# Kernel tuning notes

Measured on AMD Instinct MI355X. Metric: run time of the kernel, lower is better.

## Reference

```python
import jax, jax.numpy as jnp
import numpy as np
from jax import lax

B, H, W, C = 16, 256, 256, 1
LOC_C = 31            # channels out of localization network
BN_EPS = 1e-3         # Keras BatchNormalization default epsilon
NEG_SLOPE = 0.1       # LeakyReLU slope


def _conv_relu(x, k, b):
    y = lax.conv_general_dilated(x, k, (1, 1), 'SAME',
                                 dimension_numbers=('NHWC', 'HWIO', 'NHWC'))
    return jax.nn.relu(y + b)


def _maxpool2(x):
    return lax.reduce_window(x, -jnp.inf, lax.max, (1, 2, 2, 1), (1, 2, 2, 1), 'VALID')


def _resize_nearest(x, out_h, out_w):
    # tf.image.resize(..., method='nearest') with half-pixel centers
    b, h, w, c = x.shape
    ih = jnp.floor((jnp.arange(out_h) + 0.5) * h / out_h).astype(jnp.int32)
    iw = jnp.floor((jnp.arange(out_w) + 0.5) * w / out_w).astype(jnp.int32)
    return x[:, ih][:, :, iw]


def _generate_grid(theta, height, width):
    # base grid in [-1, 1], x varies along width, y along height
    xs = jnp.arange(width, dtype=jnp.float32) / (width - 1) * 2.0 - 1.0
    ys = jnp.arange(height, dtype=jnp.float32) / (height - 1) * 2.0 - 1.0
    gx, gy = jnp.meshgrid(xs, ys)                      # (H, W)
    grid = jnp.stack([gx, gy], axis=-1).reshape(height * width, 2)  # (HW, 2)
    th = theta.reshape(-1, 2, 3)
    A = th[:, :, :2]                                   # (B, 2, 2)
    t = th[:, :, 2]                                    # (B, 2)
    # NOTE: source does grid @ A (not A @ grid) -- replicate exactly
    tg = jnp.einsum('nc,bcd->bnd', grid, A) + t[:, None, :]
    return tg.reshape(-1, height, width, 2)


def _sampler(img, grid):
    b, h, w, c = img.shape
    x = 0.5 * ((grid[..., 0] + 1.0) * (w - 1))
    y = 0.5 * ((grid[..., 1] + 1.0) * (h - 1))
    x0 = jnp.floor(x); x1 = x0 + 1.0
    y0 = jnp.floor(y); y1 = y0 + 1.0
    x0 = jnp.clip(x0, 0.0, w - 1.0); x1 = jnp.clip(x1, 0.0, w - 1.0)
    y0 = jnp.clip(y0, 0.0, h - 1.0); y1 = jnp.clip(y1, 0.0, h - 1.0)
    wa = (x1 - x) * (y1 - y)
    wb = (x1 - x) * (y - y0)
    wc = (x - x0) * (y1 - y)
    wd = (x - x0) * (y - y0)
    xi0 = x0.astype(jnp.int32); xi1 = x1.astype(jnp.int32)
    yi0 = y0.astype(jnp.int32); yi1 = y1.astype(jnp.int32)
    img_flat = img.reshape(b, h * w, c)

    def gather(yi, xi):
        idx = (yi * w + xi).reshape(b, h * w, 1)       # (B, HW, 1)
        return jnp.take_along_axis(img_flat, idx, axis=1).reshape(b, h, w, c)

    Ia = gather(yi0, xi0)
    Ib = gather(yi1, xi0)
    Ic = gather(yi0, xi1)
    Id = gather(yi1, xi1)
    return (wa[..., None] * Ia + wb[..., None] * Ib
            + wc[..., None] * Ic + wd[..., None] * Id)


def setup_inputs() -> dict:
    key = jax.random.key(0)
    ks = jax.random.split(key, 16)
    s = 0.05
    feat = (H // 8) * (W // 8) * LOC_C  # 31744 flattened localization features
    return {
        'x': jax.random.normal(ks[0], (B, H, W, C), jnp.float32),
        'conv1_k': jax.random.normal(ks[1], (3, 3, C, 8), jnp.float32) * s,
        'conv1_b': jnp.zeros((8,), jnp.float32),
        'conv2_k': jax.random.normal(ks[2], (3, 3, 8, 16), jnp.float32) * s,
        'conv2_b': jnp.zeros((16,), jnp.float32),
        'conv3_k': jax.random.normal(ks[3], (3, 3, 16, LOC_C), jnp.float32) * s,
        'conv3_b': jnp.zeros((LOC_C,), jnp.float32),
        'bn_gamma': 1.0 + 0.1 * jax.random.normal(ks[4], (feat,), jnp.float32),
        'bn_beta': 0.1 * jax.random.normal(ks[5], (feat,), jnp.float32),
        'bn_mean': jnp.zeros((feat,), jnp.float32),
        'bn_var': jnp.ones((feat,), jnp.float32),
        'd1_k': jax.random.normal(ks[6], (feat, 64), jnp.float32) * 0.01,
        'd1_b': jnp.zeros((64,), jnp.float32),
        'd2_k': jax.random.normal(ks[7], (64, 96), jnp.float32) * s,
        'd2_b': jnp.zeros((96,), jnp.float32),
        'd3_k': jax.random.normal(ks[8], (96, 6), jnp.float32) * 0.01,
        'd3_b': jnp.array([1, 0, 0, 0, 1, 0], jnp.float32),
    }


def reference(x, conv1_k, conv1_b, conv2_k, conv2_b, conv3_k, conv3_b,
              bn_gamma, bn_beta, bn_mean, bn_var,
              d1_k, d1_b, d2_k, d2_b, d3_k, d3_b):
    # localization network: (conv-relu, pool) x3 -> (B, H/8, W/8, 31)
    xi = _maxpool2(_conv_relu(x, conv1_k, conv1_b))
    xi = _maxpool2(_conv_relu(xi, conv2_k, conv2_b))
    x_intermediate = _maxpool2(_conv_relu(xi, conv3_k, conv3_b))
    # transformation parameter network (BN in inference mode, dropout = identity)
    f = x_intermediate.reshape(x.shape[0], -1)
    f = (f - bn_mean) * jax.lax.rsqrt(bn_var + BN_EPS) * bn_gamma + bn_beta
    f = jax.nn.relu(f @ d1_k + d1_b)
    f = jax.nn.relu(f @ d2_k + d2_b)
    theta = f @ d3_k + d3_b                            # (B, 6)
    grid = _generate_grid(theta, H, W)                 # (B, H, W, 2)
    loc_up = _resize_nearest(x_intermediate, H, W)     # (B, H, W, 31)
    xc = jnp.concatenate([x, loc_up], axis=-1)         # (B, H, W, 32)
    out = _sampler(xc, grid)
    return jnp.where(out >= 0, out, NEG_SLOPE * out)
```

## Files before the change

kernel.cpp:

```cpp
#include <hip/hip_runtime.h>


#define NEG_SLOPE 0.1f
#define BN_EPS 1e-3f

__global__ __launch_bounds__(256) void st_conv1(const float* __restrict__ x,
                                                const float* __restrict__ w,
                                                const float* __restrict__ bias,
                                                float* __restrict__ outA) {
    int idx = blockIdx.x * 256 + threadIdx.x;
    int px = idx & 127, py = (idx >> 7) & 127, b = idx >> 14;
    const float* xb = x + b * 65536;
    int iy0 = 2 * py - 1, ix0 = 2 * px - 1;
    float p[16];
#pragma unroll
    for (int r = 0; r < 4; ++r) {
        int iy = iy0 + r;
        bool oky = (iy >= 0) && (iy < 256);
#pragma unroll
        for (int cc = 0; cc < 4; ++cc) {
            int ix = ix0 + cc;
            bool ok = oky && (ix >= 0) && (ix < 256);
            p[r * 4 + cc] = ok ? xb[iy * 256 + ix] : 0.0f;
        }
    }
    float m[8];
#pragma unroll
    for (int co = 0; co < 8; ++co) m[co] = -1e30f;
#pragma unroll
    for (int oy = 0; oy < 2; ++oy)
#pragma unroll
        for (int ox = 0; ox < 2; ++ox) {
            float acc[8];
#pragma unroll
            for (int co = 0; co < 8; ++co) acc[co] = 0.0f;
#pragma unroll
            for (int ky = 0; ky < 3; ++ky)
#pragma unroll
                for (int kx = 0; kx < 3; ++kx) {
                    float pv = p[(oy + ky) * 4 + (ox + kx)];
                    const float* wr = w + (ky * 3 + kx) * 8;
#pragma unroll
                    for (int co = 0; co < 8; ++co)
                        acc[co] = fmaf(pv, wr[co], acc[co]);
                }
#pragma unroll
            for (int co = 0; co < 8; ++co) m[co] = fmaxf(m[co], acc[co]);
        }
    float* o = outA + idx * 8;
#pragma unroll
    for (int co = 0; co < 8; ++co) {
        float v = m[co] + bias[co];
        o[co] = v > 0.0f ? v : 0.0f;
    }
}

__global__ __launch_bounds__(256) void st_conv2(const float* __restrict__ A,
                                                const float* __restrict__ w,
                                                const float* __restrict__ bias,
                                                float* __restrict__ outB) {
    int idx = blockIdx.x * 256 + threadIdx.x;
    int half = idx & 1;
    int pixel = idx >> 1;
    int px = pixel & 63, py = (pixel >> 6) & 63, b = pixel >> 12;
    const float* Ab = A + b * 128 * 128 * 8;
    int iy0 = 2 * py - 1, ix0 = 2 * px - 1;
    int cobase = half * 8;
    float acc[4][8];
#pragma unroll
    for (int pos = 0; pos < 4; ++pos)
#pragma unroll
        for (int co = 0; co < 8; ++co) acc[pos][co] = 0.0f;

    for (int ci = 0; ci < 8; ++ci) {
        float p[16];
#pragma unroll
        for (int r = 0; r < 4; ++r) {
            int iy = iy0 + r;
            bool oky = (iy >= 0) && (iy < 128);
#pragma unroll
            for (int cc = 0; cc < 4; ++cc) {
                int ix = ix0 + cc;
                bool ok = oky && (ix >= 0) && (ix < 128);
                p[r * 4 + cc] = ok ? Ab[(iy * 128 + ix) * 8 + ci] : 0.0f;
            }
        }
#pragma unroll
        for (int ky = 0; ky < 3; ++ky)
#pragma unroll
            for (int kx = 0; kx < 3; ++kx) {
                const float* wr = w + ((ky * 3 + kx) * 8 + ci) * 16 + cobase;
                float p00 = p[ky * 4 + kx];
                float p01 = p[ky * 4 + kx + 1];
                float p10 = p[(ky + 1) * 4 + kx];
                float p11 = p[(ky + 1) * 4 + kx + 1];
#pragma unroll
                for (int co = 0; co < 8; ++co) {
                    float wv = wr[co];
                    acc[0][co] = fmaf(p00, wv, acc[0][co]);
                    acc[1][co] = fmaf(p01, wv, acc[1][co]);
                    acc[2][co] = fmaf(p10, wv, acc[2][co]);
                    acc[3][co] = fmaf(p11, wv, acc[3][co]);
                }
            }
    }
    float* o = outB + pixel * 16 + cobase;
#pragma unroll
    for (int co = 0; co < 8; ++co) {
        float m = fmaxf(fmaxf(acc[0][co], acc[1][co]),
                        fmaxf(acc[2][co], acc[3][co]));
        m += bias[cobase + co];
        o[co] = m > 0.0f ? m : 0.0f;
    }
}

__global__ __launch_bounds__(256) void st_conv3(const float* __restrict__ Bf,
                                                const float* __restrict__ w,
                                                const float* __restrict__ bias,
                                                float* __restrict__ outC) {
    int idx = blockIdx.x * 256 + threadIdx.x;
    int q = idx & 3;
    int pixel = idx >> 2;
    int ix = pixel & 63, iy = (pixel >> 6) & 63, b = pixel >> 12;
    int cobase = q * 8;
    if (cobase > 23) cobase = 23;
    const float* Bb = Bf + b * 64 * 64 * 16;
    float acc[8];
#pragma unroll
    for (int co = 0; co < 8; ++co) acc[co] = 0.0f;

    for (int ci = 0; ci < 16; ++ci) {
        float p[9];
#pragma unroll
        for (int ky = 0; ky < 3; ++ky) {
            int y = iy + ky - 1;
            bool oky = (y >= 0) && (y < 64);
#pragma unroll
            for (int kx = 0; kx < 3; ++kx) {
                int xx = ix + kx - 1;
                bool ok = oky && (xx >= 0) && (xx < 64);
                p[ky * 3 + kx] = ok ? Bb[(y * 64 + xx) * 16 + ci] : 0.0f;
            }
        }
#pragma unroll
        for (int k = 0; k < 9; ++k) {
            float pv = p[k];
            const float* wr = w + (k * 16 + ci) * 31 + cobase;
#pragma unroll
            for (int co = 0; co < 8; ++co)
                acc[co] = fmaf(pv, wr[co], acc[co]);
        }
    }
    float* o = outC + pixel * 31 + cobase;
#pragma unroll
    for (int co = 0; co < 8; ++co) {
        float v = acc[co] + bias[cobase + co];
        o[co] = v > 0.0f ? v : 0.0f;
    }
}

__global__ __launch_bounds__(256) void st_pool3(const float* __restrict__ C3,
                                                const float* __restrict__ gamma,
                                                const float* __restrict__ beta,
                                                const float* __restrict__ mean,
                                                const float* __restrict__ var,
                                                float* __restrict__ xip,
                                                float* __restrict__ fprime) {
    int idx = blockIdx.x * 256 + threadIdx.x;
    unsigned j = (unsigned)idx % 31744u;
    unsigned b = (unsigned)idx / 31744u;
    unsigned p2 = j / 31u;
    unsigned co = j - p2 * 31u;
    unsigned px = p2 & 31u, py = p2 >> 5;
    const float* Cb = C3 + b * 64 * 64 * 31;
    float m = -1e30f;
#pragma unroll
    for (int dy = 0; dy < 2; ++dy)
#pragma unroll
        for (int dx = 0; dx < 2; ++dx)
            m = fmaxf(m, Cb[((2 * py + dy) * 64 + (2 * px + dx)) * 31 + co]);
    xip[((b << 10) + p2) * 32 + 1 + co] = m;
    float sc = gamma[j] * rsqrtf(var[j] + BN_EPS);
    fprime[idx] = (m - mean[j]) * sc + beta[j];
}

__global__ __launch_bounds__(256) void st_d1(const float* __restrict__ fp,
                                             const float* __restrict__ k1,
                                             float* __restrict__ partial) {
    int o = blockIdx.x;
    int slice = blockIdx.y;
    int t = threadIdx.x;
    float acc[16];
#pragma unroll
    for (int b = 0; b < 16; ++b) acc[b] = 0.0f;
    int jend = (slice + 1) * 1984;
    for (int j = slice * 1984 + t; j < jend; j += 256) {
        float kv = k1[j * 64 + o];
#pragma unroll
        for (int b = 0; b < 16; ++b)
            acc[b] = fmaf(fp[b * 31744 + j], kv, acc[b]);
    }
#pragma unroll
    for (int b = 0; b < 16; ++b) {
        float v = acc[b];
#pragma unroll
        for (int off = 32; off > 0; off >>= 1) v += __shfl_down(v, off, 64);
        acc[b] = v;
    }
    __shared__ float red[4][16];
    int wave = t >> 6, lane = t & 63;
    if (lane == 0) {
#pragma unroll
        for (int b = 0; b < 16; ++b) red[wave][b] = acc[b];
    }
    __syncthreads();
    if (t < 16) {
        float s = red[0][t] + red[1][t] + red[2][t] + red[3][t];
        partial[(o * 16 + slice) * 16 + t] = s;
    }
}

__global__ __launch_bounds__(256) void st_d1b(const float* __restrict__ partial,
                                              const float* __restrict__ bias,
                                              float* __restrict__ h1) {
    int gid = blockIdx.x * 256 + threadIdx.x;
    int o = gid >> 4, b = gid & 15;
    float s = 0.0f;
#pragma unroll
    for (int sl = 0; sl < 16; ++sl) s += partial[(o * 16 + sl) * 16 + b];
    s += bias[o];
    h1[b * 64 + o] = s > 0.0f ? s : 0.0f;
}

__global__ __launch_bounds__(128) void st_theta(const float* __restrict__ h1,
                                                const float* __restrict__ k2,
                                                const float* __restrict__ b2,
                                                const float* __restrict__ k3,
                                                const float* __restrict__ b3,
                                                float* __restrict__ theta) {
    int b = blockIdx.x, t = threadIdx.x;
    __shared__ float h2[96];
    if (t < 96) {
        float s = b2[t];
        for (int i = 0; i < 64; ++i) s = fmaf(h1[b * 64 + i], k2[i * 96 + t], s);
        h2[t] = s > 0.0f ? s : 0.0f;
    }
    __syncthreads();
    if (t < 6) {
        float s = b3[t];
        for (int i = 0; i < 96; ++i) s = fmaf(h2[i], k3[i * 6 + t], s);
        theta[b * 6 + t] = s;
    }
}

__global__ __launch_bounds__(256) void st_sample(const float* __restrict__ x,
                                                 const float* __restrict__ xip,
                                                 const float* __restrict__ theta,
                                                 float* __restrict__ out) {
    __shared__ float smem[256 * 33];
    int t = threadIdx.x;
    int p = blockIdx.x * 256 + t;
    int ow = p & 255, oh = (p >> 8) & 255;
    int b = blockIdx.x >> 8;

    const float* th = theta + b * 6;
    float t0 = th[0], t1 = th[1], t2 = th[2], t3 = th[3], t4 = th[4], t5 = th[5];
    float gx = (float)ow * (2.0f / 255.0f) - 1.0f;
    float gy = (float)oh * (2.0f / 255.0f) - 1.0f;
    float sx = gx * t0 + gy * t3 + t2;
    float sy = gx * t1 + gy * t4 + t5;
    float xf = 0.5f * ((sx + 1.0f) * 255.0f);
    float yf = 0.5f * ((sy + 1.0f) * 255.0f);
    float x0 = floorf(xf), y0 = floorf(yf);
    float x1 = x0 + 1.0f, y1 = y0 + 1.0f;
    x0 = fminf(fmaxf(x0, 0.0f), 255.0f);
    x1 = fminf(fmaxf(x1, 0.0f), 255.0f);
    y0 = fminf(fmaxf(y0, 0.0f), 255.0f);
    y1 = fminf(fmaxf(y1, 0.0f), 255.0f);
    float wa = (x1 - xf) * (y1 - yf);
    float wb = (x1 - xf) * (yf - y0);
    float wc = (xf - x0) * (y1 - yf);
    float wd = (xf - x0) * (yf - y0);
    int xi0 = (int)x0, xi1 = (int)x1, yi0 = (int)y0, yi1 = (int)y1;

    const float* xb = x + b * 65536;
    float Ia = xb[yi0 * 256 + xi0];
    float Ib = xb[yi1 * 256 + xi0];
    float Ic = xb[yi0 * 256 + xi1];
    float Id = xb[yi1 * 256 + xi1];
    float fine = wa * Ia + wb * Ib + wc * Ic + wd * Id;
    fine = fine >= 0.0f ? fine : NEG_SLOPE * fine;

    const float* cellbase = xip + (b << 15);
    const float4* pa = (const float4*)(cellbase + (((yi0 >> 3) << 5) + (xi0 >> 3)) * 32);
    const float4* pb = (const float4*)(cellbase + (((yi1 >> 3) << 5) + (xi0 >> 3)) * 32);
    const float4* pc = (const float4*)(cellbase + (((yi0 >> 3) << 5) + (xi1 >> 3)) * 32);
    const float4* pd = (const float4*)(cellbase + (((yi1 >> 3) << 5) + (xi1 >> 3)) * 32);

    int sbase = t * 33;
#pragma unroll
    for (int k = 0; k < 8; ++k) {
        float4 va = pa[k], vb = pb[k], vc = pc[k], vd = pd[k];
        float vx = fmaf(wa, va.x, fmaf(wb, vb.x, fmaf(wc, vc.x, wd * vd.x)));
        float vy = fmaf(wa, va.y, fmaf(wb, vb.y, fmaf(wc, vc.y, wd * vd.y)));
        float vz = fmaf(wa, va.z, fmaf(wb, vb.z, fmaf(wc, vc.z, wd * vd.z)));
        float vw = fmaf(wa, va.w, fmaf(wb, vb.w, fmaf(wc, vc.w, wd * vd.w)));
        vx = vx >= 0.0f ? vx : NEG_SLOPE * vx;
        vy = vy >= 0.0f ? vy : NEG_SLOPE * vy;
        vz = vz >= 0.0f ? vz : NEG_SLOPE * vz;
        vw = vw >= 0.0f ? vw : NEG_SLOPE * vw;
        if (k == 0) vx = fine;
        smem[sbase + 4 * k]     = vx;
        smem[sbase + 4 * k + 1] = vy;
        smem[sbase + 4 * k + 2] = vz;
        smem[sbase + 4 * k + 3] = vw;
    }
    __syncthreads();

    float* ob = out + blockIdx.x * 8192;
#pragma unroll
    for (int i = 0; i < 32; ++i) {
        int idx = i * 256 + t;
        ob[idx] = smem[(idx >> 5) * 33 + (idx & 31)];
    }
}

extern "C" void kernel_launch(void* const* d_in, const int* in_sizes, int n_in,
                              void* d_out, int out_size, void* d_ws, size_t ws_size,
                              hipStream_t stream) {
    const float* x     = (const float*)d_in[0];
    const float* c1k   = (const float*)d_in[1];
    const float* c1b   = (const float*)d_in[2];
    const float* c2k   = (const float*)d_in[3];
    const float* c2b   = (const float*)d_in[4];
    const float* c3k   = (const float*)d_in[5];
    const float* c3b   = (const float*)d_in[6];
    const float* gamma = (const float*)d_in[7];
    const float* beta  = (const float*)d_in[8];
    const float* mean  = (const float*)d_in[9];
    const float* var   = (const float*)d_in[10];
    const float* d1k   = (const float*)d_in[11];
    const float* d1b   = (const float*)d_in[12];
    const float* d2k   = (const float*)d_in[13];
    const float* d2b   = (const float*)d_in[14];
    const float* d3k   = (const float*)d_in[15];
    const float* d3b   = (const float*)d_in[16];
    float* out = (float*)d_out;
    float* ws  = (float*)d_ws;

    float* A       = ws;
    float* Bf      = ws + 2097152;
    float* C3      = ws;
    float* xip     = ws + 2097152;
    float* fprime  = ws + 2097152 + 524288;
    float* partial = ws + 3145728;
    float* h1      = ws + 3145728 + 16384;
    float* theta   = ws + 3145728 + 17408;

    st_conv1<<<1024, 256, 0, stream>>>(x, c1k, c1b, A);
    st_conv2<<<512, 256, 0, stream>>>(A, c2k, c2b, Bf);
    st_conv3<<<1024, 256, 0, stream>>>(Bf, c3k, c3b, C3);
    st_pool3<<<1984, 256, 0, stream>>>(C3, gamma, beta, mean, var, xip, fprime);
    st_d1<<<dim3(64, 16), 256, 0, stream>>>(fprime, d1k, partial);
    st_d1b<<<4, 256, 0, stream>>>(partial, d1b, h1);
    st_theta<<<16, 128, 0, stream>>>(h1, d2k, d2b, d3k, d3b, theta);
    st_sample<<<4096, 256, 0, stream>>>(x, xip, theta, out);
}
```

Before: 309.4 us.

## Vectorize conv and pool loads, pad conv3 output, restructure dense1 and sampler stores

```diff
diff --git a/kernel.cpp b/kernel.cpp
--- a/kernel.cpp
+++ b/kernel.cpp
@@ -4,10 +4,18 @@
 #define NEG_SLOPE 0.1f
 #define BN_EPS 1e-3f
 
-__global__ __launch_bounds__(256) void st_conv1(const float* __restrict__ x,
-                                                const float* __restrict__ w,
-                                                const float* __restrict__ bias,
-                                                float* __restrict__ outA) {
+typedef float vfloat4 __attribute__((ext_vector_type(4)));
+
+__device__ __forceinline__ void fma8(float pv, const float* __restrict__ wk,
+                                     float* __restrict__ acc) {
+#pragma unroll
+    for (int co = 0; co < 8; ++co) acc[co] = fmaf(pv, wk[co], acc[co]);
+}
+
+__global__ __launch_bounds__(256, 4) void st_conv1(const float* __restrict__ x,
+                                                   const float* __restrict__ w,
+                                                   const float* __restrict__ bias,
+                                                   float* __restrict__ outA) {
     int idx = blockIdx.x * 256 + threadIdx.x;
     int px = idx & 127, py = (idx >> 7) & 127, b = idx >> 14;
     const float* xb = x + b * 65536;
@@ -37,31 +45,30 @@
 #pragma unroll
             for (int ky = 0; ky < 3; ++ky)
 #pragma unroll
-                for (int kx = 0; kx < 3; ++kx) {
-                    float pv = p[(oy + ky) * 4 + (ox + kx)];
-                    const float* wr = w + (ky * 3 + kx) * 8;
-#pragma unroll
-                    for (int co = 0; co < 8; ++co)
-                        acc[co] = fmaf(pv, wr[co], acc[co]);
-                }
+                for (int kx = 0; kx < 3; ++kx)
+                    fma8(p[(oy + ky) * 4 + (ox + kx)], w + (ky * 3 + kx) * 8, acc);
 #pragma unroll
             for (int co = 0; co < 8; ++co) m[co] = fmaxf(m[co], acc[co]);
         }
-    float* o = outA + idx * 8;
-#pragma unroll
-    for (int co = 0; co < 8; ++co) {
-        float v = m[co] + bias[co];
-        o[co] = v > 0.0f ? v : 0.0f;
-    }
-}
-
-__global__ __launch_bounds__(256) void st_conv2(const float* __restrict__ A,
-                                                const float* __restrict__ w,
-                                                const float* __restrict__ bias,
-                                                float* __restrict__ outB) {
-    int idx = blockIdx.x * 256 + threadIdx.x;
-    int half = idx & 1;
-    int pixel = idx >> 1;
+    float4 o0, o1;
+    float r0 = m[0] + bias[0], r1 = m[1] + bias[1], r2 = m[2] + bias[2], r3 = m[3] + bias[3];
+    float r4 = m[4] + bias[4], r5 = m[5] + bias[5], r6 = m[6] + bias[6], r7 = m[7] + bias[7];
+    o0.x = r0 > 0.f ? r0 : 0.f; o0.y = r1 > 0.f ? r1 : 0.f;
+    o0.z = r2 > 0.f ? r2 : 0.f; o0.w = r3 > 0.f ? r3 : 0.f;
+    o1.x = r4 > 0.f ? r4 : 0.f; o1.y = r5 > 0.f ? r5 : 0.f;
+    o1.z = r6 > 0.f ? r6 : 0.f; o1.w = r7 > 0.f ? r7 : 0.f;
+    *(float4*)(outA + idx * 8) = o0;
+    *(float4*)(outA + idx * 8 + 4) = o1;
+}
+
+__global__ __launch_bounds__(256, 2) void st_conv2(const float* __restrict__ A,
+                                                   const float* __restrict__ w,
+                                                   const float* __restrict__ bias,
+                                                   float* __restrict__ outB) {
+    int t = threadIdx.x;
+    int lane = t & 63;
+    int half = __builtin_amdgcn_readfirstlane((t >> 6) & 1);
+    int pixel = blockIdx.x * 128 + ((t >> 7) << 6) + lane;
     int px = pixel & 63, py = (pixel >> 6) & 63, b = pixel >> 12;
     const float* Ab = A + b * 128 * 128 * 8;
     int iy0 = 2 * py - 1, ix0 = 2 * px - 1;
@@ -72,8 +79,10 @@
 #pragma unroll
         for (int co = 0; co < 8; ++co) acc[pos][co] = 0.0f;
 
-    for (int ci = 0; ci < 8; ++ci) {
-        float p[16];
+    const float4 z4 = {0.f, 0.f, 0.f, 0.f};
+#pragma unroll
+    for (int ciq = 0; ciq < 2; ++ciq) {
+        float4 p[16];
 #pragma unroll
         for (int r = 0; r < 4; ++r) {
             int iy = iy0 + r;
@@ -82,27 +91,26 @@
             for (int cc = 0; cc < 4; ++cc) {
                 int ix = ix0 + cc;
                 bool ok = oky && (ix >= 0) && (ix < 128);
-                p[r * 4 + cc] = ok ? Ab[(iy * 128 + ix) * 8 + ci] : 0.0f;
+                p[r * 4 + cc] = ok ? *(const float4*)(Ab + ((iy * 128 + ix) * 8 + ciq * 4))
+                                   : z4;
             }
         }
 #pragma unroll
-        for (int ky = 0; ky < 3; ++ky)
-#pragma unroll
-            for (int kx = 0; kx < 3; ++kx) {
-                const float* wr = w + ((ky * 3 + kx) * 8 + ci) * 16 + cobase;
-                float p00 = p[ky * 4 + kx];
-                float p01 = p[ky * 4 + kx + 1];
-                float p10 = p[(ky + 1) * 4 + kx];
-                float p11 = p[(ky + 1) * 4 + kx + 1];
-#pragma unroll
-                for (int co = 0; co < 8; ++co) {
-                    float wv = wr[co];
-                    acc[0][co] = fmaf(p00, wv, acc[0][co]);
-                    acc[1][co] = fmaf(p01, wv, acc[1][co]);
-                    acc[2][co] = fmaf(p10, wv, acc[2][co]);
-                    acc[3][co] = fmaf(p11, wv, acc[3][co]);
-                }
-            }
+        for (int oy = 0; oy < 2; ++oy)
+#pragma unroll
+            for (int ox = 0; ox < 2; ++ox)
+#pragma unroll
+                for (int ky = 0; ky < 3; ++ky)
+#pragma unroll
+                    for (int kx = 0; kx < 3; ++kx) {
+                        float4 pv = p[(oy + ky) * 4 + (ox + kx)];
+                        const float* wk = w + ((ky * 3 + kx) * 8 + ciq * 4) * 16 + cobase;
+                        float* a = acc[oy * 2 + ox];
+                        fma8(pv.x, wk, a);
+                        fma8(pv.y, wk + 16, a);
+                        fma8(pv.z, wk + 32, a);
+                        fma8(pv.w, wk + 48, a);
+                    }
     }
     float* o = outB + pixel * 16 + cobase;
 #pragma unroll
@@ -114,23 +122,26 @@
     }
 }
 
-__global__ __launch_bounds__(256) void st_conv3(const float* __restrict__ Bf,
-                                                const float* __restrict__ w,
-                                                const float* __restrict__ bias,
-                                                float* __restrict__ outC) {
-    int idx = blockIdx.x * 256 + threadIdx.x;
-    int q = idx & 3;
-    int pixel = idx >> 2;
-    int ix = pixel & 63, iy = (pixel >> 6) & 63, b = pixel >> 12;
+__global__ __launch_bounds__(256, 4) void st_conv3(const float* __restrict__ Bf,
+                                                   const float* __restrict__ w,
+                                                   const float* __restrict__ bias,
+                                                   float* __restrict__ outC) {
+    int t = threadIdx.x;
+    int lane = t & 63;
+    int q = __builtin_amdgcn_readfirstlane(t >> 6);
     int cobase = q * 8;
     if (cobase > 23) cobase = 23;
+    int pixel = blockIdx.x * 64 + lane;
+    int ix = pixel & 63, iy = (pixel >> 6) & 63, b = pixel >> 12;
     const float* Bb = Bf + b * 64 * 64 * 16;
     float acc[8];
 #pragma unroll
     for (int co = 0; co < 8; ++co) acc[co] = 0.0f;
 
-    for (int ci = 0; ci < 16; ++ci) {
-        float p[9];
+    const float4 z4 = {0.f, 0.f, 0.f, 0.f};
+#pragma unroll
+    for (int ciq = 0; ciq < 4; ++ciq) {
+        float4 p[9];
 #pragma unroll
         for (int ky = 0; ky < 3; ++ky) {
             int y = iy + ky - 1;
@@ -139,19 +150,21 @@
             for (int kx = 0; kx < 3; ++kx) {
                 int xx = ix + kx - 1;
                 bool ok = oky && (xx >= 0) && (xx < 64);
-                p[ky * 3 + kx] = ok ? Bb[(y * 64 + xx) * 16 + ci] : 0.0f;
+                p[ky * 3 + kx] = ok ? *(const float4*)(Bb + ((y * 64 + xx) * 16 + ciq * 4))
+                                    : z4;
             }
         }
 #pragma unroll
         for (int k = 0; k < 9; ++k) {
-            float pv = p[k];
-            const float* wr = w + (k * 16 + ci) * 31 + cobase;
-#pragma unroll
-            for (int co = 0; co < 8; ++co)
-                acc[co] = fmaf(pv, wr[co], acc[co]);
-        }
-    }
-    float* o = outC + pixel * 31 + cobase;
+            float4 pv = p[k];
+            const float* wk = w + (k * 16 + ciq * 4) * 31 + cobase;
+            fma8(pv.x, wk, acc);
+            fma8(pv.y, wk + 31, acc);
+            fma8(pv.z, wk + 62, acc);
+            fma8(pv.w, wk + 93, acc);
+        }
+    }
+    float* o = outC + pixel * 32 + cobase;
 #pragma unroll
     for (int co = 0; co < 8; ++co) {
         float v = acc[co] + bias[cobase + co];
@@ -159,7 +172,7 @@
     }
 }
 
-__global__ __launch_bounds__(256) void st_pool3(const float* __restrict__ C3,
+__global__ __launch_bounds__(256) void st_pool3(const float* __restrict__ C3p,
                                                 const float* __restrict__ gamma,
                                                 const float* __restrict__ beta,
                                                 const float* __restrict__ mean,
@@ -167,56 +180,65 @@
                                                 float* __restrict__ xip,
                                                 float* __restrict__ fprime) {
     int idx = blockIdx.x * 256 + threadIdx.x;
-    unsigned j = (unsigned)idx % 31744u;
-    unsigned b = (unsigned)idx / 31744u;
-    unsigned p2 = j / 31u;
-    unsigned co = j - p2 * 31u;
-    unsigned px = p2 & 31u, py = p2 >> 5;
-    const float* Cb = C3 + b * 64 * 64 * 31;
-    float m = -1e30f;
-#pragma unroll
-    for (int dy = 0; dy < 2; ++dy)
-#pragma unroll
-        for (int dx = 0; dx < 2; ++dx)
-            m = fmaxf(m, Cb[((2 * py + dy) * 64 + (2 * px + dx)) * 31 + co]);
-    xip[((b << 10) + p2) * 32 + 1 + co] = m;
-    float sc = gamma[j] * rsqrtf(var[j] + BN_EPS);
-    fprime[idx] = (m - mean[j]) * sc + beta[j];
+    int quad = idx & 7;
+    int pp = idx >> 3;
+    int b = pp >> 10;
+    int cell = pp & 1023;
+    int py = cell >> 5, px = cell & 31;
+    const float* Cb = C3p + (b * 4096) * 32 + quad * 4;
+    float4 v00 = *(const float4*)(Cb + ((2 * py) * 64 + 2 * px) * 32);
+    float4 v01 = *(const float4*)(Cb + ((2 * py) * 64 + 2 * px + 1) * 32);
+    float4 v10 = *(const float4*)(Cb + ((2 * py + 1) * 64 + 2 * px) * 32);
+    float4 v11 = *(const float4*)(Cb + ((2 * py + 1) * 64 + 2 * px + 1) * 32);
+    float4 m;
+    m.x = fmaxf(fmaxf(v00.x, v01.x), fmaxf(v10.x, v11.x));
+    m.y = fmaxf(fmaxf(v00.y, v01.y), fmaxf(v10.y, v11.y));
+    m.z = fmaxf(fmaxf(v00.z, v01.z), fmaxf(v10.z, v11.z));
+    m.w = fmaxf(fmaxf(v00.w, v01.w), fmaxf(v10.w, v11.w));
+    *(float4*)(xip + (b * 1024 + cell) * 32 + quad * 4) = m;
+    int c0 = quad * 4;
+    float mv[4] = {m.x, m.y, m.z, m.w};
+#pragma unroll
+    for (int c = 0; c < 4; ++c) {
+        int co = c0 + c;
+        if (co < 31) {
+            int j = cell * 31 + co;
+            float sc = gamma[j] * rsqrtf(var[j] + BN_EPS);
+            fprime[b * 31744 + j] = (mv[c] - mean[j]) * sc + beta[j];
+        }
+    }
 }
 
 __global__ __launch_bounds__(256) void st_d1(const float* __restrict__ fp,
                                              const float* __restrict__ k1,
                                              float* __restrict__ partial) {
-    int o = blockIdx.x;
-    int slice = blockIdx.y;
-    int t = threadIdx.x;
+    int t = threadIdx.x, s = blockIdx.x;
+    int o = t & 63;
+    int sub = t >> 6;
+    int subu = __builtin_amdgcn_readfirstlane(sub);
+    int j0 = s * 124 + subu * 31;
     float acc[16];
 #pragma unroll
     for (int b = 0; b < 16; ++b) acc[b] = 0.0f;
-    int jend = (slice + 1) * 1984;
-    for (int j = slice * 1984 + t; j < jend; j += 256) {
+#pragma unroll 4
+    for (int jj = 0; jj < 31; ++jj) {
+        int j = j0 + jj;
         float kv = k1[j * 64 + o];
+        const float* fpj = fp + j;
 #pragma unroll
         for (int b = 0; b < 16; ++b)
-            acc[b] = fmaf(fp[b * 31744 + j], kv, acc[b]);
-    }
-#pragma unroll
-    for (int b = 0; b < 16; ++b) {
-        float v = acc[b];
-#pragma unroll
-        for (int off = 32; off > 0; off >>= 1) v += __shfl_down(v, off, 64);
-        acc[b] = v;
-    }
-    __shared__ float red[4][16];
-    int wave = t >> 6, lane = t & 63;
-    if (lane == 0) {
-#pragma unroll
-        for (int b = 0; b < 16; ++b) red[wave][b] = acc[b];
-    }
+            acc[b] = fmaf(fpj[b * 31744], kv, acc[b]);
+    }
+    __shared__ float red[4][16][64];
+#pragma unroll
+    for (int b = 0; b < 16; ++b) red[sub][b][o] = acc[b];
     __syncthreads();
-    if (t < 16) {
-        float s = red[0][t] + red[1][t] + red[2][t] + red[3][t];
-        partial[(o * 16 + slice) * 16 + t] = s;
+    if (sub == 0) {
+#pragma unroll
+        for (int b = 0; b < 16; ++b) {
+            float v = red[0][b][o] + red[1][b][o] + red[2][b][o] + red[3][b][o];
+            partial[(s * 64 + o) * 16 + b] = v;
+        }
     }
 }
 
@@ -226,8 +248,8 @@
     int gid = blockIdx.x * 256 + threadIdx.x;
     int o = gid >> 4, b = gid & 15;
     float s = 0.0f;
-#pragma unroll
-    for (int sl = 0; sl < 16; ++sl) s += partial[(o * 16 + sl) * 16 + b];
+#pragma unroll 8
+    for (int sl = 0; sl < 256; ++sl) s += partial[(sl * 64 + o) * 16 + b];
     s += bias[o];
     h1[b * 64 + o] = s > 0.0f ? s : 0.0f;
 }
@@ -253,11 +275,11 @@
     }
 }
 
-__global__ __launch_bounds__(256) void st_sample(const float* __restrict__ x,
-                                                 const float* __restrict__ xip,
-                                                 const float* __restrict__ theta,
-                                                 float* __restrict__ out) {
-    __shared__ float smem[256 * 33];
+__global__ __launch_bounds__(256, 4) void st_sample(const float* __restrict__ x,
+                                                    const float* __restrict__ xip,
+                                                    const float* __restrict__ theta,
+                                                    float* __restrict__ out) {
+    __shared__ float smem[256 * 34];
     int t = threadIdx.x;
     int p = blockIdx.x * 256 + t;
     int ow = p & 255, oh = (p >> 8) & 255;
@@ -297,7 +319,8 @@
     const float4* pc = (const float4*)(cellbase + (((yi0 >> 3) << 5) + (xi1 >> 3)) * 32);
     const float4* pd = (const float4*)(cellbase + (((yi1 >> 3) << 5) + (xi1 >> 3)) * 32);
 
-    int sbase = t * 33;
+    int sbase = t * 34;
+    smem[sbase] = fine;
 #pragma unroll
     for (int k = 0; k < 8; ++k) {
         float4 va = pa[k], vb = pb[k], vc = pc[k], vd = pd[k];
@@ -309,19 +332,22 @@
         vy = vy >= 0.0f ? vy : NEG_SLOPE * vy;
         vz = vz >= 0.0f ? vz : NEG_SLOPE * vz;
         vw = vw >= 0.0f ? vw : NEG_SLOPE * vw;
-        if (k == 0) vx = fine;
-        smem[sbase + 4 * k]     = vx;
-        smem[sbase + 4 * k + 1] = vy;
-        smem[sbase + 4 * k + 2] = vz;
-        smem[sbase + 4 * k + 3] = vw;
+        smem[sbase + 1 + 4 * k]     = vx;
+        smem[sbase + 2 + 4 * k]     = vy;
+        smem[sbase + 3 + 4 * k]     = vz;
+        smem[sbase + 4 + 4 * k]     = vw;
     }
     __syncthreads();
 
-    float* ob = out + blockIdx.x * 8192;
-#pragma unroll
-    for (int i = 0; i < 32; ++i) {
-        int idx = i * 256 + t;
-        ob[idx] = smem[(idx >> 5) * 33 + (idx & 31)];
+    vfloat4* ob = (vfloat4*)(out + blockIdx.x * 8192);
+#pragma unroll
+    for (int i = 0; i < 8; ++i) {
+        int g = i * 256 + t;
+        int row = g >> 3, col = 4 * (g & 7);
+        float2 lo = *(const float2*)&smem[row * 34 + col];
+        float2 hi = *(const float2*)&smem[row * 34 + col + 2];
+        vfloat4 v = {lo.x, lo.y, hi.x, hi.y};
+        __builtin_nontemporal_store(v, ob + g);
     }
 }
 
@@ -350,18 +376,18 @@
 
     float* A       = ws;
     float* Bf      = ws + 2097152;
-    float* C3      = ws;
+    float* C3p     = ws;
     float* xip     = ws + 2097152;
-    float* fprime  = ws + 2097152 + 524288;
-    float* partial = ws + 3145728;
-    float* h1      = ws + 3145728 + 16384;
-    float* theta   = ws + 3145728 + 17408;
+    float* fprime  = ws + 3145728;
+    float* partial = ws + 3653632;
+    float* h1      = ws + 3915776;
+    float* theta   = ws + 3916800;
 
     st_conv1<<<1024, 256, 0, stream>>>(x, c1k, c1b, A);
     st_conv2<<<512, 256, 0, stream>>>(A, c2k, c2b, Bf);
-    st_conv3<<<1024, 256, 0, stream>>>(Bf, c3k, c3b, C3);
-    st_pool3<<<1984, 256, 0, stream>>>(C3, gamma, beta, mean, var, xip, fprime);
-    st_d1<<<dim3(64, 16), 256, 0, stream>>>(fprime, d1k, partial);
+    st_conv3<<<1024, 256, 0, stream>>>(Bf, c3k, c3b, C3p);
+    st_pool3<<<512, 256, 0, stream>>>(C3p, gamma, beta, mean, var, xip, fprime);
+    st_d1<<<256, 256, 0, stream>>>(fprime, d1k, partial);
     st_d1b<<<4, 256, 0, stream>>>(partial, d1b, h1);
     st_theta<<<16, 128, 0, stream>>>(h1, d2k, d2b, d3k, d3b, theta);
     st_sample<<<4096, 256, 0, stream>>>(x, xip, theta, out);
```

New measurement: 279.4 us. 1.11x faster.
